# Kernel optimization log

Hardware: AMD Instinct MI355X
Metric: run time of the kernel (lower is better)

## Reference

```python
import jax, jax.numpy as jnp
import numpy as np

GAMMA = 1.0 / 512.0  # RBF bandwidth, 1/d_feat


def _rbf_kernel(X, Z, gamma):
    # X: [N, d], Z: [M, d] -> K: [N, M], K[i,j] = exp(-gamma * ||x_i - z_j||^2)
    xn = jnp.sum(X * X, axis=1, keepdims=True)        # [N, 1]
    zn = jnp.sum(Z * Z, axis=1, keepdims=True).T      # [1, M]
    sq = xn + zn - 2.0 * (X @ Z.T)                    # [N, M]
    return jnp.exp(-gamma * jnp.maximum(sq, 0.0))


def setup_inputs() -> dict:
    key = jax.random.key(0)
    k1, k2, k3, k4, k5 = jax.random.split(key, 5)
    N, d, M = 8192, 512, 4096
    inputs = jax.random.normal(k1, (M, d), dtype=jnp.float32)
    X = jax.random.normal(k2, (N, d), dtype=jnp.float32)
    # SVM labels in {-1, +1}
    Y = jnp.where(jax.random.uniform(k3, (N, 1)) > 0.5, 1.0, -1.0).astype(jnp.float32)
    a = jax.random.normal(k4, (N, 1), dtype=jnp.float32) * 0.1
    b = jax.random.normal(k5, (1, 1), dtype=jnp.float32)
    return {"inputs": inputs, "X": X, "Y": Y, "a": a, "b": b}


def reference(inputs, X, Y, a, b):
    # K: [N, M]; weighted sum over support vectors N, then add bias, transpose.
    K = _rbf_kernel(X, inputs, GAMMA)                 # [N, M]
    s = jnp.sum(a * Y * K, axis=0)                    # [M]
    out = (s + b)                                     # [1, M] via broadcast with [1,1]
    return out.T                                      # [M, 1]
```

## Files before the change

### kernel.cpp

```cpp
#include <hip/hip_runtime.h>
#include <hip/hip_bf16.h>
#include <stdint.h>

#define C2EXP (-0.0028179443441958f)

static constexpr int N_SV = 8192;
static constexpr int M_Q  = 4096;
static constexpr int DIM  = 512;
static constexpr int NP_A = N_SV / 16;
static constexpr int NP_B = M_Q / 16;
static constexpr int NKT  = DIM / 32;

typedef __bf16 bf16x8 __attribute__((ext_vector_type(8)));
typedef float  f32x4  __attribute__((ext_vector_type(4)));

#define GLB const __attribute__((address_space(1))) void
#define LDS __attribute__((address_space(3))) void

__global__ __launch_bounds__(256) void svm_prep(
    const float* __restrict__ Z, const float* __restrict__ X,
    const float* __restrict__ Y, const float* __restrict__ a,
    const float* __restrict__ b,
    __bf16* __restrict__ Xp, __bf16* __restrict__ Zp,
    float* __restrict__ xn, float* __restrict__ zn, float* __restrict__ w,
    float* __restrict__ out)
{
    __shared__ float part[4][16];

    const int tid  = threadIdx.x;
    const int lane = tid & 63;
    const int wv   = tid >> 6;
    const int pb   = blockIdx.x;
    const bool isA = (pb < NP_A);
    const int p    = isA ? pb : pb - NP_A;
    const float* src = (isA ? X : Z) + (size_t)p * 16 * DIM;
    __bf16* dst  = isA ? Xp : Zp;
    const int np = isA ? NP_A : NP_B;

    const int row = lane & 15;
    const int ch  = lane >> 4;

    float s = 0.0f;
    #pragma unroll
    for (int f = 0; f < 4; ++f) {
        const int kt = wv * 4 + f;
        const float4* rp = (const float4*)(src + (size_t)row * DIM + kt * 32 + ch * 8);
        float4 v0 = rp[0], v1 = rp[1];
        s += v0.x*v0.x + v0.y*v0.y + v0.z*v0.z + v0.w*v0.w
           + v1.x*v1.x + v1.y*v1.y + v1.z*v1.z + v1.w*v1.w;
        __bf16 h[8] = {(__bf16)v0.x, (__bf16)v0.y, (__bf16)v0.z, (__bf16)v0.w,
                       (__bf16)v1.x, (__bf16)v1.y, (__bf16)v1.z, (__bf16)v1.w};
        uint4 bits;
        __builtin_memcpy(&bits, h, 16);
        *(uint4*)((char*)dst + (((size_t)kt * np + p) << 10) + lane * 16) = bits;
    }

    s += __shfl_xor(s, 16);
    s += __shfl_xor(s, 32);
    if (lane < 16) part[wv][lane] = s;
    __syncthreads();

    if (tid < 16) {
        const float t = part[0][tid] + part[1][tid] + part[2][tid] + part[3][tid];
        const int r = p * 16 + tid;
        if (isA) { xn[r] = t; w[r] = a[r] * Y[r]; }
        else     { zn[r] = t; out[r] = b[0]; }
    }
}

__global__ __launch_bounds__(512, 2) void svm_main(
    const __bf16* __restrict__ Xp, const __bf16* __restrict__ Zp,
    const float* __restrict__ xn, const float* __restrict__ zn,
    const float* __restrict__ w, float* __restrict__ out)
{
    __shared__ char Sh[65536];

    const int tid  = threadIdx.x;
    const int lane = tid & 63;
    const int wid  = tid >> 6;
    const int wr   = wid >> 2;
    const int wc   = wid & 3;

    const int iBase = blockIdx.y * 256;
    const int jBase = blockIdx.x * 256;
    const int pbA   = blockIdx.y * 16;
    const int pbB   = blockIdx.x * 16;

    f32x4 acc[8][4];
    #pragma unroll
    for (int m = 0; m < 8; ++m)
        #pragma unroll
        for (int n = 0; n < 4; ++n)
            acc[m][n] = (f32x4)(0.0f);

    auto stage = [&](const __bf16* Mp, int pb16, int t, int op, int np) {
        char* dst0 = (char*)Sh + ((t & 1) * 32768) + op * 16384 + tid * 16;
        const char* s0 = (const char*)Mp + (((size_t)t * np + pb16) << 10) + tid * 16;
        __builtin_amdgcn_global_load_lds((GLB*)s0, (LDS*)dst0, 16, 0, 0);
        __builtin_amdgcn_global_load_lds((GLB*)(s0 + 8192), (LDS*)(dst0 + 8192),
                                         16, 0, 0);
    };

    stage(Xp, pbA, 0, 0, NP_A);
    stage(Zp, pbB, 0, 1, NP_B);
    stage(Zp, pbB, 1, 1, NP_B);
    asm volatile("s_waitcnt vmcnt(2)" ::: "memory");
    __builtin_amdgcn_s_barrier();

    bf16x8 af[4], bfr[4];

    #pragma unroll
    for (int t = 0; t < NKT; ++t) {
        const int buf = t & 1;
        const char* Ab = (const char*)Sh + buf * 32768 + lane * 16;

        #pragma unroll
        for (int m = 0; m < 4; ++m)
            af[m] = *(const bf16x8*)(Ab + (wr * 8 + m) * 1024);
        #pragma unroll
        for (int n = 0; n < 4; ++n)
            bfr[n] = *(const bf16x8*)(Ab + 16384 + (wc * 4 + n) * 1024);
        if (t + 1 < NKT) stage(Xp, pbA, t + 1, 0, NP_A);
        __builtin_amdgcn_s_barrier();
        asm volatile("s_waitcnt lgkmcnt(0)" ::: "memory");
        __builtin_amdgcn_sched_barrier(0);
        __builtin_amdgcn_s_setprio(1);
        #pragma unroll
        for (int m = 0; m < 4; ++m)
            #pragma unroll
            for (int n = 0; n < 4; ++n)
                acc[m][n] = __builtin_amdgcn_mfma_f32_16x16x32_bf16(
                    af[m], bfr[n], acc[m][n], 0, 0, 0);
        __builtin_amdgcn_s_setprio(0);
        __builtin_amdgcn_s_barrier();

        #pragma unroll
        for (int m = 0; m < 4; ++m)
            af[m] = *(const bf16x8*)(Ab + (wr * 8 + 4 + m) * 1024);
        if (t + 2 < NKT) stage(Zp, pbB, t + 2, 1, NP_B);
        __builtin_amdgcn_s_barrier();
        asm volatile("s_waitcnt lgkmcnt(0)" ::: "memory");
        __builtin_amdgcn_sched_barrier(0);
        __builtin_amdgcn_s_setprio(1);
        #pragma unroll
        for (int m = 0; m < 4; ++m)
            #pragma unroll
            for (int n = 0; n < 4; ++n)
                acc[4 + m][n] = __builtin_amdgcn_mfma_f32_16x16x32_bf16(
                    af[m], bfr[n], acc[4 + m][n], 0, 0, 0);
        __builtin_amdgcn_s_setprio(0);

        if (t < NKT - 2) {
            asm volatile("s_waitcnt vmcnt(2)" ::: "memory");
            __builtin_amdgcn_s_barrier();
        } else if (t == NKT - 2) {
            asm volatile("s_waitcnt vmcnt(0)" ::: "memory");
            __builtin_amdgcn_s_barrier();
        }
    }

    const int rg   = lane >> 4;
    const int lcol = lane & 15;

    float znv[4];
    #pragma unroll
    for (int n = 0; n < 4; ++n)
        znv[n] = zn[jBase + wc * 64 + n * 16 + lcol];

    float cs[4] = {0.f, 0.f, 0.f, 0.f};
    #pragma unroll
    for (int m = 0; m < 8; ++m) {
        float wv[4], xv[4];
        #pragma unroll
        for (int r = 0; r < 4; ++r) {
            const int i = iBase + wr * 128 + m * 16 + rg * 4 + r;
            wv[r] = w[i];
            xv[r] = xn[i];
        }
        #pragma unroll
        for (int n = 0; n < 4; ++n)
            #pragma unroll
            for (int r = 0; r < 4; ++r) {
                float d = xv[r] + znv[n] - 2.0f * acc[m][n][r];
                d = fmaxf(d, 0.0f);
                cs[n] += wv[r] * exp2f(C2EXP * d);
            }
    }

    #pragma unroll
    for (int n = 0; n < 4; ++n) {
        const int j = jBase + wc * 64 + n * 16 + lcol;
        float c = cs[n];
        c += __shfl_xor(c, 16);
        c += __shfl_xor(c, 32);
        if (lane < 16) atomicAdd(out + j, c);
    }
}

extern "C" void kernel_launch(void* const* d_in, const int* in_sizes, int n_in,
                              void* d_out, int out_size, void* d_ws, size_t ws_size,
                              hipStream_t stream)
{
    const float* Z = (const float*)d_in[0];
    const float* X = (const float*)d_in[1];
    const float* Y = (const float*)d_in[2];
    const float* a = (const float*)d_in[3];
    const float* b = (const float*)d_in[4];
    float* out = (float*)d_out;

    char* ws = (char*)d_ws;
    __bf16* Xp = (__bf16*)ws;
    __bf16* Zp = (__bf16*)(ws + 8ull * 1024 * 1024);
    float*  xn = (float*)(ws + 12ull * 1024 * 1024);
    float*  zn = xn + N_SV;
    float*  w  = zn + M_Q;

    svm_prep<<<NP_A + NP_B, 256, 0, stream>>>(Z, X, Y, a, b, Xp, Zp, xn, zn, w, out);
    svm_main<<<dim3(M_Q / 256, N_SV / 256), 512, 0, stream>>>(Xp, Zp, xn, zn, w, out);
}
```

Baseline: 111.3 us.

## Split main loop into four MFMA phases with half-tile prefetch two steps ahead

The k-loop now runs four smaller MFMA phases, each using 4x2 fragments instead of two phases using 4x4 fragments. Each stage call loads a half tile, and both operands are prefetched two k-steps ahead into the buffer just drained, so global-to-LDS traffic is spread across more barrier points. The prep kernel permutes the 16-row panel order inside each 256-row tile so every phase reads contiguous LDS panels while the epilogue row and column mapping stays correct. The goal is better overlap of memory loads with MFMA work and a smaller B-fragment register footprint. The cost is twice as many barriers per iteration and tighter vmcnt bookkeeping.

```diff
diff --git a/kernel.cpp b/kernel.cpp
--- a/kernel.cpp
+++ b/kernel.cpp
@@ -36,6 +36,12 @@
     const float* src = (isA ? X : Z) + (size_t)p * 16 * DIM;
     __bf16* dst  = isA ? Xp : Zp;
     const int np = isA ? NP_A : NP_B;
+
+    const int q    = p & 15;
+    const int tile = p >> 4;
+    const int slot = isA ? (((q >> 2) & 1) * 8 + (q >> 3) * 4 + (q & 3))
+                         : (((q >> 1) & 1) * 8 + (q >> 2) * 2 + (q & 1));
+    const size_t stIdx = (size_t)tile * 16 + slot;
 
     const int row = lane & 15;
     const int ch  = lane >> 4;
@@ -52,7 +58,7 @@
                        (__bf16)v1.x, (__bf16)v1.y, (__bf16)v1.z, (__bf16)v1.w};
         uint4 bits;
         __builtin_memcpy(&bits, h, 16);
-        *(uint4*)((char*)dst + (((size_t)kt * np + p) << 10) + lane * 16) = bits;
+        *(uint4*)((char*)dst + (((size_t)kt * np + stIdx) << 10) + lane * 16) = bits;
     }
 
     s += __shfl_xor(s, 16);
@@ -93,70 +99,108 @@
         for (int n = 0; n < 4; ++n)
             acc[m][n] = (f32x4)(0.0f);
 
-    auto stage = [&](const __bf16* Mp, int pb16, int t, int op, int np) {
-        char* dst0 = (char*)Sh + ((t & 1) * 32768) + op * 16384 + tid * 16;
-        const char* s0 = (const char*)Mp + (((size_t)t * np + pb16) << 10) + tid * 16;
-        __builtin_amdgcn_global_load_lds((GLB*)s0, (LDS*)dst0, 16, 0, 0);
-        __builtin_amdgcn_global_load_lds((GLB*)(s0 + 8192), (LDS*)(dst0 + 8192),
-                                         16, 0, 0);
+    auto stageH = [&](const __bf16* Mp, int pb16, int kt, int op, int h, int np) {
+        char* dst = (char*)Sh + (kt & 1) * 32768 + op * 16384 + h * 8192 + tid * 16;
+        const char* s0 = (const char*)Mp + (((size_t)kt * np + pb16) << 10)
+                       + h * 8192 + tid * 16;
+        __builtin_amdgcn_global_load_lds((GLB*)s0, (LDS*)dst, 16, 0, 0);
     };
 
-    stage(Xp, pbA, 0, 0, NP_A);
-    stage(Zp, pbB, 0, 1, NP_B);
-    stage(Zp, pbB, 1, 1, NP_B);
-    asm volatile("s_waitcnt vmcnt(2)" ::: "memory");
+    stageH(Xp, pbA, 0, 0, 0, NP_A);
+    stageH(Xp, pbA, 0, 0, 1, NP_A);
+    stageH(Zp, pbB, 0, 1, 0, NP_B);
+    stageH(Zp, pbB, 0, 1, 1, NP_B);
+    stageH(Xp, pbA, 1, 0, 0, NP_A);
+    stageH(Xp, pbA, 1, 0, 1, NP_A);
+    stageH(Zp, pbB, 1, 1, 0, NP_B);
+    stageH(Zp, pbB, 1, 1, 1, NP_B);
+    asm volatile("s_waitcnt vmcnt(4)" ::: "memory");
     __builtin_amdgcn_s_barrier();
 
-    bf16x8 af[4], bfr[4];
+    bf16x8 af[4], bf[4];
 
     #pragma unroll
     for (int t = 0; t < NKT; ++t) {
         const int buf = t & 1;
         const char* Ab = (const char*)Sh + buf * 32768 + lane * 16;
-
-        #pragma unroll
-        for (int m = 0; m < 4; ++m)
-            af[m] = *(const bf16x8*)(Ab + (wr * 8 + m) * 1024);
-        #pragma unroll
-        for (int n = 0; n < 4; ++n)
-            bfr[n] = *(const bf16x8*)(Ab + 16384 + (wc * 4 + n) * 1024);
-        if (t + 1 < NKT) stage(Xp, pbA, t + 1, 0, NP_A);
-        __builtin_amdgcn_s_barrier();
-        asm volatile("s_waitcnt lgkmcnt(0)" ::: "memory");
-        __builtin_amdgcn_sched_barrier(0);
-        __builtin_amdgcn_s_setprio(1);
-        #pragma unroll
-        for (int m = 0; m < 4; ++m)
-            #pragma unroll
-            for (int n = 0; n < 4; ++n)
-                acc[m][n] = __builtin_amdgcn_mfma_f32_16x16x32_bf16(
-                    af[m], bfr[n], acc[m][n], 0, 0, 0);
-        __builtin_amdgcn_s_setprio(0);
-        __builtin_amdgcn_s_barrier();
-
-        #pragma unroll
-        for (int m = 0; m < 4; ++m)
-            af[m] = *(const bf16x8*)(Ab + (wr * 8 + 4 + m) * 1024);
-        if (t + 2 < NKT) stage(Zp, pbB, t + 2, 1, NP_B);
-        __builtin_amdgcn_s_barrier();
-        asm volatile("s_waitcnt lgkmcnt(0)" ::: "memory");
-        __builtin_amdgcn_sched_barrier(0);
-        __builtin_amdgcn_s_setprio(1);
-        #pragma unroll
-        for (int m = 0; m < 4; ++m)
-            #pragma unroll
-            for (int n = 0; n < 4; ++n)
-                acc[4 + m][n] = __builtin_amdgcn_mfma_f32_16x16x32_bf16(
-                    af[m], bfr[n], acc[4 + m][n], 0, 0, 0);
-        __builtin_amdgcn_s_setprio(0);
-
+        const char* Bb = Ab + 16384;
+
+        #pragma unroll
+        for (int mi = 0; mi < 4; ++mi)
+            af[mi] = *(const bf16x8*)(Ab + (wr * 4 + mi) * 1024);
+        #pragma unroll
+        for (int j = 0; j < 2; ++j)
+            bf[j] = *(const bf16x8*)(Bb + (wc * 2 + j) * 1024);
+        __builtin_amdgcn_s_barrier();
+        asm volatile("s_waitcnt lgkmcnt(0)" ::: "memory");
+        __builtin_amdgcn_sched_barrier(0);
+        __builtin_amdgcn_s_setprio(1);
+        #pragma unroll
+        for (int mi = 0; mi < 4; ++mi)
+            #pragma unroll
+            for (int n = 0; n < 2; ++n)
+                acc[mi][n] = __builtin_amdgcn_mfma_f32_16x16x32_bf16(
+                    af[mi], bf[n], acc[mi][n], 0, 0, 0);
+        __builtin_amdgcn_s_setprio(0);
+        __builtin_amdgcn_s_barrier();
+
+        #pragma unroll
+        for (int j = 0; j < 2; ++j)
+            bf[2 + j] = *(const bf16x8*)(Bb + (8 + wc * 2 + j) * 1024);
+        if (t + 2 < NKT) {
+            stageH(Xp, pbA, t + 2, 0, 0, NP_A);
+            stageH(Zp, pbB, t + 2, 1, 0, NP_B);
+        }
+        __builtin_amdgcn_s_barrier();
+        asm volatile("s_waitcnt lgkmcnt(0)" ::: "memory");
+        __builtin_amdgcn_sched_barrier(0);
+        __builtin_amdgcn_s_setprio(1);
+        #pragma unroll
+        for (int mi = 0; mi < 4; ++mi)
+            #pragma unroll
+            for (int n = 2; n < 4; ++n)
+                acc[mi][n] = __builtin_amdgcn_mfma_f32_16x16x32_bf16(
+                    af[mi], bf[n], acc[mi][n], 0, 0, 0);
+        __builtin_amdgcn_s_setprio(0);
+        __builtin_amdgcn_s_barrier();
+
+        #pragma unroll
+        for (int mi = 0; mi < 4; ++mi)
+            af[mi] = *(const bf16x8*)(Ab + (8 + wr * 4 + mi) * 1024);
+        if (t + 2 < NKT)
+            stageH(Zp, pbB, t + 2, 1, 1, NP_B);
+        __builtin_amdgcn_s_barrier();
+        asm volatile("s_waitcnt lgkmcnt(0)" ::: "memory");
+        __builtin_amdgcn_sched_barrier(0);
+        __builtin_amdgcn_s_setprio(1);
+        #pragma unroll
+        for (int mi = 0; mi < 4; ++mi)
+            #pragma unroll
+            for (int n = 0; n < 2; ++n)
+                acc[4 + mi][n] = __builtin_amdgcn_mfma_f32_16x16x32_bf16(
+                    af[mi], bf[n], acc[4 + mi][n], 0, 0, 0);
+        __builtin_amdgcn_s_setprio(0);
+        __builtin_amdgcn_s_barrier();
+
+        if (t + 2 < NKT)
+            stageH(Xp, pbA, t + 2, 0, 1, NP_A);
+        __builtin_amdgcn_s_barrier();
+        asm volatile("s_waitcnt lgkmcnt(0)" ::: "memory");
+        __builtin_amdgcn_sched_barrier(0);
+        __builtin_amdgcn_s_setprio(1);
+        #pragma unroll
+        for (int mi = 0; mi < 4; ++mi)
+            #pragma unroll
+            for (int n = 2; n < 4; ++n)
+                acc[4 + mi][n] = __builtin_amdgcn_mfma_f32_16x16x32_bf16(
+                    af[mi], bf[n], acc[4 + mi][n], 0, 0, 0);
+        __builtin_amdgcn_s_setprio(0);
         if (t < NKT - 2) {
-            asm volatile("s_waitcnt vmcnt(2)" ::: "memory");
-            __builtin_amdgcn_s_barrier();
+            asm volatile("s_waitcnt vmcnt(4)" ::: "memory");
         } else if (t == NKT - 2) {
             asm volatile("s_waitcnt vmcnt(0)" ::: "memory");
-            __builtin_amdgcn_s_barrier();
         }
+        __builtin_amdgcn_s_barrier();
     }
 
     const int rg   = lane >> 4;
```

Result: no change. 113.5 us (+2.0%).
